# Optimization experiments

Hardware: AMD Instinct MI355X
Metric: run time of the kernel (lower is better)

## Reference

```python
import jax, jax.numpy as jnp
import numpy as np

B, P, N, H = 2, 512, 8, 32
INIT_RANGE = 0.02


def setup_inputs() -> dict:
    key = jax.random.key(0)
    k1, k2, k3 = jax.random.split(key, 3)
    d = jax.random.normal(k1, (B, P, N, H), dtype=jnp.float32)
    e = jax.random.normal(k2, (B, P, N, H), dtype=jnp.float32)
    W = jax.random.normal(k3, (N, H, H, H), dtype=jnp.float32) * INIT_RANGE
    return {"d": d, "e": e, "W": W}


def reference(d, e, W):
    # Trilinear contraction: v[b,p1,p2,n,h3] = sum_{h1,h2} d[b,p1,n,h1] e[b,p2,n,h2] W[n,h1,h2,h3]
    # Decompose into two batched matmuls to avoid the naive 4-way product:
    # tmp[b,p1,n,h2,h3] = sum_h1 d[b,p1,n,h1] W[n,h1,h2,h3]
    tmp = jnp.einsum('bpni,nijk->bpnjk', d, W)
    # v[b,p1,p2,n,h3] = sum_h2 tmp[b,p1,n,h2,h3] e[b,p2,n,h2]
    v = jnp.einsum('bpnjk,bqnj->bpqnk', tmp, e)
    return v
```

## Files before the change

kernel.cpp:

```cpp
#include <hip/hip_runtime.h>

#define BB 2
#define PP 512
#define NN 8
#define HH 32

typedef float f4     __attribute__((ext_vector_type(4)));
typedef float f32x4  __attribute__((ext_vector_type(4)));
typedef short bf16x8 __attribute__((ext_vector_type(8)));

__device__ __forceinline__ short f2bf(float f) {
  union { float f; unsigned u; } v; v.f = f;
  unsigned r = v.u + 0x7FFFu + ((v.u >> 16) & 1u);
  return (short)(r >> 16);
}

__global__ __launch_bounds__(256) void prep_kernel(
    const float* __restrict__ d, const float* __restrict__ W,
    short* __restrict__ tmpT) {
  const int bid    = blockIdx.x;
  const int b      = bid >> 9;
  const int rem    = bid & 511;
  const int n      = rem >> 6;
  const int p1base = (rem & 63) * 8;
  const int t      = threadIdx.x;

  __shared__ float dT[32][8];
  {
    const int h1 = t & 31, p1l = t >> 5;
    dT[h1][p1l] = d[(size_t)((b * PP + p1base + p1l) * NN + n) * HH + h1];
  }
  __syncthreads();

  const float* Wn = W + (size_t)n * HH * HH * HH;
  #pragma unroll
  for (int pp = 0; pp < 4; ++pp) {
    const int q  = pp * 256 + t;
    const int h3 = q & 31;
    const int h2 = q >> 5;
    float acc[8] = {0.f, 0.f, 0.f, 0.f, 0.f, 0.f, 0.f, 0.f};
    for (int h1 = 0; h1 < 32; ++h1) {
      const float w = Wn[h1 * 1024 + h2 * 32 + h3];
      const f4 a0 = *(const f4*)&dT[h1][0];
      const f4 a1 = *(const f4*)&dT[h1][4];
      acc[0] = fmaf(a0[0], w, acc[0]);
      acc[1] = fmaf(a0[1], w, acc[1]);
      acc[2] = fmaf(a0[2], w, acc[2]);
      acc[3] = fmaf(a0[3], w, acc[3]);
      acc[4] = fmaf(a1[0], w, acc[4]);
      acc[5] = fmaf(a1[1], w, acc[5]);
      acc[6] = fmaf(a1[2], w, acc[6]);
      acc[7] = fmaf(a1[3], w, acc[7]);
    }
    const size_t obase =
        ((size_t)(b * PP + p1base) * NN + n) * (HH * HH) + h3 * 32 + h2;
    #pragma unroll
    for (int p1l = 0; p1l < 8; ++p1l)
      tmpT[obase + (size_t)p1l * (NN * HH * HH)] = f2bf(acc[p1l]);
  }
}

__global__ __launch_bounds__(256) void ecvt_kernel(
    const float* __restrict__ e, short* __restrict__ eB) {
  const int i = (blockIdx.x * 256 + threadIdx.x) * 8;
  const f4 e0 = *(const f4*)(e + i);
  const f4 e1 = *(const f4*)(e + i + 4);
  bf16x8 v;
  v[0] = f2bf(e0[0]); v[1] = f2bf(e0[1]); v[2] = f2bf(e0[2]); v[3] = f2bf(e0[3]);
  v[4] = f2bf(e1[0]); v[5] = f2bf(e1[1]); v[6] = f2bf(e1[2]); v[7] = f2bf(e1[3]);
  *(bf16x8*)(eB + i) = v;
}

__global__ __launch_bounds__(256, 4) void vmain_kernel(
    const short* __restrict__ eB, const short* __restrict__ tmpT,
    float* __restrict__ out) {
  const int bid = blockIdx.x;
  const int b   = bid >> 9;
  const int p1  = bid & 511;
  const int t   = threadIdx.x;
  const int wv  = t >> 6;
  const int l   = t & 63;
  const int lr  = l & 15;
  const int lk  = l >> 4;

  bf16x8 bfr[8][2];
  const short* tb = tmpT + (size_t)(b * PP + p1) * (NN * HH * HH);
  #pragma unroll
  for (int n = 0; n < 8; ++n)
    #pragma unroll
    for (int c = 0; c < 2; ++c)
      bfr[n][c] = *(const bf16x8*)(tb + n * (HH * HH) + (c * 16 + lr) * 32 + lk * 8);

  const short* ebb  = eB + (size_t)b * (PP * NN * HH);
  float*       outb = out + (size_t)(b * PP + p1) * (PP * NN * HH);
  const f32x4  z    = {0.f, 0.f, 0.f, 0.f};

  for (int i = 0; i < 8; ++i) {
    const int m0 = (wv * 8 + i) * 16;
    #pragma unroll
    for (int n = 0; n < 8; ++n) {
      const bf16x8 a =
          *(const bf16x8*)(ebb + (size_t)((m0 + lr) * NN + n) * HH + lk * 8);
      const f32x4 c0 = __builtin_amdgcn_mfma_f32_16x16x32_bf16(bfr[n][0], a, z, 0, 0, 0);
      const f32x4 c1 = __builtin_amdgcn_mfma_f32_16x16x32_bf16(bfr[n][1], a, z, 0, 0, 0);
      float* op = outb + (size_t)(m0 + lr) * (NN * HH) + n * HH + lk * 4;
      *(f32x4*)op        = c0;
      *(f32x4*)(op + 16) = c1;
    }
  }
}

__device__ __forceinline__ void gemm_pv_f32e(const bf16x8 (&bfr)[8][2],
                                             const float* __restrict__ eb,
                                             float* __restrict__ outb,
                                             int wv, int lr, int lk) {
  for (int i = 0; i < 8; ++i) {
    const int m0 = (wv * 8 + i) * 16;
    #pragma unroll
    for (int n = 0; n < 8; ++n) {
      const float* ep = eb + (size_t)(((m0 + lr) * NN + n) * HH + lk * 8);
      const f4 e0 = *(const f4*)ep;
      const f4 e1 = *(const f4*)(ep + 4);
      bf16x8 a;
      a[0] = f2bf(e0[0]); a[1] = f2bf(e0[1]); a[2] = f2bf(e0[2]); a[3] = f2bf(e0[3]);
      a[4] = f2bf(e1[0]); a[5] = f2bf(e1[1]); a[6] = f2bf(e1[2]); a[7] = f2bf(e1[3]);
      const f32x4 z = {0.f, 0.f, 0.f, 0.f};
      const f32x4 c0 = __builtin_amdgcn_mfma_f32_16x16x32_bf16(bfr[n][0], a, z, 0, 0, 0);
      const f32x4 c1 = __builtin_amdgcn_mfma_f32_16x16x32_bf16(bfr[n][1], a, z, 0, 0, 0);
      float* op = outb + (size_t)(m0 + lr) * (NN * HH) + n * HH + lk * 4;
      *(f32x4*)op        = c0;
      *(f32x4*)(op + 16) = c1;
    }
  }
}

__global__ __launch_bounds__(256, 4) void fused_kernel(
    const float* __restrict__ d, const float* __restrict__ e,
    const float* __restrict__ W, float* __restrict__ out) {
  const int bid = blockIdx.x;
  const int b   = bid >> 9;
  const int p1  = bid & 511;
  const int t   = threadIdx.x;

  __shared__ float dsh[NN * HH];
  __shared__ short tsh[NN * HH * HH];
  dsh[t] = d[(size_t)(b * PP + p1) * (NN * HH) + t];
  __syncthreads();

  const int h3  = t & 31;
  const int h2b = t >> 5;
  for (int n = 0; n < 8; ++n) {
    f4 dv[8];
    #pragma unroll
    for (int j = 0; j < 8; ++j) dv[j] = *(const f4*)&dsh[n * 32 + j * 4];
    const float* Wn = W + (size_t)n * (HH * HH * HH);
    #pragma unroll
    for (int h2s = 0; h2s < 4; ++h2s) {
      const int h2 = h2s * 8 + h2b;
      float acc = 0.f;
      #pragma unroll
      for (int j = 0; j < 8; ++j)
        #pragma unroll
        for (int k = 0; k < 4; ++k)
          acc = fmaf(dv[j][k], Wn[(j * 4 + k) * 1024 + h2 * 32 + h3], acc);
      tsh[n * 1024 + h3 * 32 + h2] = f2bf(acc);
    }
  }
  __syncthreads();

  const int wv = t >> 6;
  const int l  = t & 63;
  const int lr = l & 15;
  const int lk = l >> 4;
  bf16x8 bfr[8][2];
  #pragma unroll
  for (int n = 0; n < 8; ++n)
    #pragma unroll
    for (int c = 0; c < 2; ++c)
      bfr[n][c] = *(const bf16x8*)&tsh[n * (HH * HH) + (c * 16 + lr) * 32 + lk * 8];

  gemm_pv_f32e(bfr, e + (size_t)b * (PP * NN * HH),
               out + (size_t)(b * PP + p1) * (PP * NN * HH), wv, lr, lk);
}

extern "C" void kernel_launch(void* const* d_in, const int* in_sizes, int n_in,
                              void* d_out, int out_size, void* d_ws, size_t ws_size,
                              hipStream_t stream) {
  const float* d = (const float*)d_in[0];
  const float* e = (const float*)d_in[1];
  const float* W = (const float*)d_in[2];
  float* out = (float*)d_out;

  const size_t tmp_bytes = (size_t)BB * PP * NN * HH * HH * sizeof(short);
  const size_t eb_bytes  = (size_t)BB * PP * NN * HH * sizeof(short);
  if (ws_size >= tmp_bytes + eb_bytes) {
    short* tmpT = (short*)d_ws;
    short* eB   = (short*)((char*)d_ws + tmp_bytes);
    prep_kernel<<<dim3(BB * NN * (PP / 8)), dim3(256), 0, stream>>>(d, W, tmpT);
    ecvt_kernel<<<dim3(BB * PP * NN * HH / (256 * 8)), dim3(256), 0, stream>>>(e, eB);
    vmain_kernel<<<dim3(BB * PP), dim3(256), 0, stream>>>(eB, tmpT, out);
  } else {
    fused_kernel<<<dim3(BB * PP), dim3(256), 0, stream>>>(d, e, W, out);
  }
}
```

Measured before the change: 151.3 us.

## Register-tile tmp precompute with transposed W and stage output stores through LDS

Adds a kernel that transposes W per (n,h1) slice so the tmp precompute can read eight contiguous h2 weights at once. Each thread then computes an 8x8 register tile (8 p1 values by 8 h2 values) and writes packed bf16x8 results instead of scattered 2-byte stores. The main MFMA kernel now stages its outputs through a swizzled LDS buffer, so each row is written to global memory as contiguous 512-byte segments rather than strided 16-byte chunks. In exchange it adds an extra launch, a larger workspace requirement, and extra LDS use that may lower occupancy.

```diff
diff --git a/kernel.cpp b/kernel.cpp
--- a/kernel.cpp
+++ b/kernel.cpp
@@ -15,48 +15,83 @@
   return (short)(r >> 16);
 }
 
-__global__ __launch_bounds__(256) void prep_kernel(
-    const float* __restrict__ d, const float* __restrict__ W,
+__global__ __launch_bounds__(256) void wtrans_kernel(
+    const float* __restrict__ W, float* __restrict__ WT) {
+  const int blk = blockIdx.x;
+  const int t   = threadIdx.x;
+  __shared__ float ls[32][33];
+  const float* src = W  + (size_t)blk * 1024;
+  float*       dst = WT + (size_t)blk * 1024;
+  #pragma unroll
+  for (int r = 0; r < 4; ++r) {
+    const int h2 = r * 8 + (t >> 5), h3 = t & 31;
+    ls[h2][h3] = src[h2 * 32 + h3];
+  }
+  __syncthreads();
+  #pragma unroll
+  for (int r = 0; r < 4; ++r) {
+    const int h3 = r * 8 + (t >> 5), h2 = t & 31;
+    dst[h3 * 32 + h2] = ls[h2][h3];
+  }
+}
+
+__global__ __launch_bounds__(256) void prep2_kernel(
+    const float* __restrict__ d, const float* __restrict__ WT,
     short* __restrict__ tmpT) {
   const int bid    = blockIdx.x;
-  const int b      = bid >> 9;
-  const int rem    = bid & 511;
-  const int n      = rem >> 6;
+  const int b      = bid >> 8;
+  const int rem    = bid & 255;
+  const int npair  = rem >> 6;
   const int p1base = (rem & 63) * 8;
   const int t      = threadIdx.x;
 
-  __shared__ float dT[32][8];
+  __shared__ float dsh[2][32][8];
   {
-    const int h1 = t & 31, p1l = t >> 5;
-    dT[h1][p1l] = d[(size_t)((b * PP + p1base + p1l) * NN + n) * HH + h1];
-  }
-  __syncthreads();
-
-  const float* Wn = W + (size_t)n * HH * HH * HH;
-  #pragma unroll
-  for (int pp = 0; pp < 4; ++pp) {
-    const int q  = pp * 256 + t;
-    const int h3 = q & 31;
-    const int h2 = q >> 5;
-    float acc[8] = {0.f, 0.f, 0.f, 0.f, 0.f, 0.f, 0.f, 0.f};
-    for (int h1 = 0; h1 < 32; ++h1) {
-      const float w = Wn[h1 * 1024 + h2 * 32 + h3];
-      const f4 a0 = *(const f4*)&dT[h1][0];
-      const f4 a1 = *(const f4*)&dT[h1][4];
-      acc[0] = fmaf(a0[0], w, acc[0]);
-      acc[1] = fmaf(a0[1], w, acc[1]);
-      acc[2] = fmaf(a0[2], w, acc[2]);
-      acc[3] = fmaf(a0[3], w, acc[3]);
-      acc[4] = fmaf(a1[0], w, acc[4]);
-      acc[5] = fmaf(a1[1], w, acc[5]);
-      acc[6] = fmaf(a1[2], w, acc[6]);
-      acc[7] = fmaf(a1[3], w, acc[7]);
-    }
-    const size_t obase =
-        ((size_t)(b * PP + p1base) * NN + n) * (HH * HH) + h3 * 32 + h2;
-    #pragma unroll
-    for (int p1l = 0; p1l < 8; ++p1l)
-      tmpT[obase + (size_t)p1l * (NN * HH * HH)] = f2bf(acc[p1l]);
+    const int h1 = t & 31, p1l = (t >> 5) & 7;
+    #pragma unroll
+    for (int r = 0; r < 2; ++r)
+      dsh[r][h1][p1l] =
+          d[(size_t)((b * PP + p1base + p1l) * NN + npair * 2 + r) * HH + h1];
+  }
+  __syncthreads();
+
+  const int np  = t >> 7;
+  const int h3  = (t >> 2) & 31;
+  const int h2g = t & 3;
+  const int n   = npair * 2 + np;
+
+  float acc[8][8];
+  #pragma unroll
+  for (int p = 0; p < 8; ++p)
+    #pragma unroll
+    for (int q = 0; q < 8; ++q) acc[p][q] = 0.f;
+
+  const float* wb = WT + ((size_t)(n * HH) * HH + h3) * HH + h2g * 8;
+  for (int h1 = 0; h1 < 32; ++h1) {
+    const f4 w0 = *(const f4*)(wb + (size_t)h1 * 1024);
+    const f4 w1 = *(const f4*)(wb + (size_t)h1 * 1024 + 4);
+    const f4 d0 = *(const f4*)&dsh[np][h1][0];
+    const f4 d1 = *(const f4*)&dsh[np][h1][4];
+    #pragma unroll
+    for (int p = 0; p < 4; ++p) {
+      #pragma unroll
+      for (int q = 0; q < 4; ++q) {
+        acc[p][q]         = fmaf(d0[p], w0[q], acc[p][q]);
+        acc[p][q + 4]     = fmaf(d0[p], w1[q], acc[p][q + 4]);
+        acc[p + 4][q]     = fmaf(d1[p], w0[q], acc[p + 4][q]);
+        acc[p + 4][q + 4] = fmaf(d1[p], w1[q], acc[p + 4][q + 4]);
+      }
+    }
+  }
+
+  const size_t obase =
+      ((size_t)(b * PP + p1base) * NN + n) * (HH * HH) + h3 * 32 + h2g * 8;
+  #pragma unroll
+  for (int p = 0; p < 8; ++p) {
+    bf16x8 v;
+    #pragma unroll
+    for (int q = 0; q < 8; ++q) v[q] = f2bf(acc[p][q]);
+    *(bf16x8*)(tmpT + obase + (size_t)p * (NN * HH * HH)) = v;
   }
 }
 
@@ -83,6 +118,9 @@
   const int lr  = l & 15;
   const int lk  = l >> 4;
 
+  __shared__ float lbuf[4][16][128];
+  float* wl = &lbuf[wv][0][0];
+
   bf16x8 bfr[8][2];
   const short* tb = tmpT + (size_t)(b * PP + p1) * (NN * HH * HH);
   #pragma unroll
@@ -98,22 +136,79 @@
   for (int i = 0; i < 8; ++i) {
     const int m0 = (wv * 8 + i) * 16;
     #pragma unroll
-    for (int n = 0; n < 8; ++n) {
-      const bf16x8 a =
-          *(const bf16x8*)(ebb + (size_t)((m0 + lr) * NN + n) * HH + lk * 8);
-      const f32x4 c0 = __builtin_amdgcn_mfma_f32_16x16x32_bf16(bfr[n][0], a, z, 0, 0, 0);
-      const f32x4 c1 = __builtin_amdgcn_mfma_f32_16x16x32_bf16(bfr[n][1], a, z, 0, 0, 0);
-      float* op = outb + (size_t)(m0 + lr) * (NN * HH) + n * HH + lk * 4;
-      *(f32x4*)op        = c0;
-      *(f32x4*)(op + 16) = c1;
-    }
-  }
-}
-
-__device__ __forceinline__ void gemm_pv_f32e(const bf16x8 (&bfr)[8][2],
-                                             const float* __restrict__ eb,
-                                             float* __restrict__ outb,
-                                             int wv, int lr, int lk) {
+    for (int half = 0; half < 2; ++half) {
+      const int n0 = half * 4;
+      #pragma unroll
+      for (int nn = 0; nn < 4; ++nn) {
+        const int n = n0 + nn;
+        const bf16x8 a =
+            *(const bf16x8*)(ebb + (size_t)((m0 + lr) * NN + n) * HH + lk * 8);
+        const f32x4 c0 = __builtin_amdgcn_mfma_f32_16x16x32_bf16(bfr[n][0], a, z, 0, 0, 0);
+        const f32x4 c1 = __builtin_amdgcn_mfma_f32_16x16x32_bf16(bfr[n][1], a, z, 0, 0, 0);
+        const int s0 = (nn * 8 + lk)     ^ (lr & 7);
+        const int s1 = (nn * 8 + 4 + lk) ^ (lr & 7);
+        *(f32x4*)(wl + lr * 128 + s0 * 4) = c0;
+        *(f32x4*)(wl + lr * 128 + s1 * 4) = c1;
+      }
+      #pragma unroll
+      for (int j = 0; j < 8; ++j) {
+        const int row  = 2 * j + (l >> 5);
+        const int slot = l & 31;
+        const f32x4 v = *(const f32x4*)(wl + row * 128 + ((slot ^ (row & 7)) * 4));
+        *(f32x4*)(outb + (size_t)(m0 + row) * (NN * HH) + n0 * HH + slot * 4) = v;
+      }
+    }
+  }
+}
+
+__global__ __launch_bounds__(256, 4) void fused_kernel(
+    const float* __restrict__ d, const float* __restrict__ e,
+    const float* __restrict__ W, float* __restrict__ out) {
+  const int bid = blockIdx.x;
+  const int b   = bid >> 9;
+  const int p1  = bid & 511;
+  const int t   = threadIdx.x;
+
+  __shared__ float dsh[NN * HH];
+  __shared__ short tsh[NN * HH * HH];
+  dsh[t] = d[(size_t)(b * PP + p1) * (NN * HH) + t];
+  __syncthreads();
+
+  const int h3  = t & 31;
+  const int h2b = t >> 5;
+  for (int n = 0; n < 8; ++n) {
+    f4 dv[8];
+    #pragma unroll
+    for (int j = 0; j < 8; ++j) dv[j] = *(const f4*)&dsh[n * 32 + j * 4];
+    const float* Wn = W + (size_t)n * (HH * HH * HH);
+    #pragma unroll
+    for (int h2s = 0; h2s < 4; ++h2s) {
+      const int h2 = h2s * 8 + h2b;
+      float acc = 0.f;
+      #pragma unroll
+      for (int j = 0; j < 8; ++j)
+        #pragma unroll
+        for (int k = 0; k < 4; ++k)
+          acc = fmaf(dv[j][k], Wn[(j * 4 + k) * 1024 + h2 * 32 + h3], acc);
+      tsh[n * 1024 + h3 * 32 + h2] = f2bf(acc);
+    }
+  }
+  __syncthreads();
+
+  const int wv = t >> 6;
+  const int l  = t & 63;
+  const int lr = l & 15;
+  const int lk = l >> 4;
+  bf16x8 bfr[8][2];
+  #pragma unroll
+  for (int n = 0; n < 8; ++n)
+    #pragma unroll
+    for (int c = 0; c < 2; ++c)
+      bfr[n][c] = *(const bf16x8*)&tsh[n * (HH * HH) + (c * 16 + lr) * 32 + lk * 8];
+
+  const float* eb   = e + (size_t)b * (PP * NN * HH);
+  float*       outb = out + (size_t)(b * PP + p1) * (PP * NN * HH);
+  const f32x4  z    = {0.f, 0.f, 0.f, 0.f};
   for (int i = 0; i < 8; ++i) {
     const int m0 = (wv * 8 + i) * 16;
     #pragma unroll
@@ -124,7 +219,6 @@
       bf16x8 a;
       a[0] = f2bf(e0[0]); a[1] = f2bf(e0[1]); a[2] = f2bf(e0[2]); a[3] = f2bf(e0[3]);
       a[4] = f2bf(e1[0]); a[5] = f2bf(e1[1]); a[6] = f2bf(e1[2]); a[7] = f2bf(e1[3]);
-      const f32x4 z = {0.f, 0.f, 0.f, 0.f};
       const f32x4 c0 = __builtin_amdgcn_mfma_f32_16x16x32_bf16(bfr[n][0], a, z, 0, 0, 0);
       const f32x4 c1 = __builtin_amdgcn_mfma_f32_16x16x32_bf16(bfr[n][1], a, z, 0, 0, 0);
       float* op = outb + (size_t)(m0 + lr) * (NN * HH) + n * HH + lk * 4;
@@ -132,55 +226,6 @@
       *(f32x4*)(op + 16) = c1;
     }
   }
-}
-
-__global__ __launch_bounds__(256, 4) void fused_kernel(
-    const float* __restrict__ d, const float* __restrict__ e,
-    const float* __restrict__ W, float* __restrict__ out) {
-  const int bid = blockIdx.x;
-  const int b   = bid >> 9;
-  const int p1  = bid & 511;
-  const int t   = threadIdx.x;
-
-  __shared__ float dsh[NN * HH];
-  __shared__ short tsh[NN * HH * HH];
-  dsh[t] = d[(size_t)(b * PP + p1) * (NN * HH) + t];
-  __syncthreads();
-
-  const int h3  = t & 31;
-  const int h2b = t >> 5;
-  for (int n = 0; n < 8; ++n) {
-    f4 dv[8];
-    #pragma unroll
-    for (int j = 0; j < 8; ++j) dv[j] = *(const f4*)&dsh[n * 32 + j * 4];
-    const float* Wn = W + (size_t)n * (HH * HH * HH);
-    #pragma unroll
-    for (int h2s = 0; h2s < 4; ++h2s) {
-      const int h2 = h2s * 8 + h2b;
-      float acc = 0.f;
-      #pragma unroll
-      for (int j = 0; j < 8; ++j)
-        #pragma unroll
-        for (int k = 0; k < 4; ++k)
-          acc = fmaf(dv[j][k], Wn[(j * 4 + k) * 1024 + h2 * 32 + h3], acc);
-      tsh[n * 1024 + h3 * 32 + h2] = f2bf(acc);
-    }
-  }
-  __syncthreads();
-
-  const int wv = t >> 6;
-  const int l  = t & 63;
-  const int lr = l & 15;
-  const int lk = l >> 4;
-  bf16x8 bfr[8][2];
-  #pragma unroll
-  for (int n = 0; n < 8; ++n)
-    #pragma unroll
-    for (int c = 0; c < 2; ++c)
-      bfr[n][c] = *(const bf16x8*)&tsh[n * (HH * HH) + (c * 16 + lr) * 32 + lk * 8];
-
-  gemm_pv_f32e(bfr, e + (size_t)b * (PP * NN * HH),
-               out + (size_t)(b * PP + p1) * (PP * NN * HH), wv, lr, lk);
 }
 
 extern "C" void kernel_launch(void* const* d_in, const int* in_sizes, int n_in,
@@ -193,11 +238,14 @@
 
   const size_t tmp_bytes = (size_t)BB * PP * NN * HH * HH * sizeof(short);
   const size_t eb_bytes  = (size_t)BB * PP * NN * HH * sizeof(short);
-  if (ws_size >= tmp_bytes + eb_bytes) {
+  const size_t wt_bytes  = (size_t)NN * HH * HH * HH * sizeof(float);
+  if (ws_size >= tmp_bytes + eb_bytes + wt_bytes) {
     short* tmpT = (short*)d_ws;
     short* eB   = (short*)((char*)d_ws + tmp_bytes);
-    prep_kernel<<<dim3(BB * NN * (PP / 8)), dim3(256), 0, stream>>>(d, W, tmpT);
+    float* WT   = (float*)((char*)d_ws + tmp_bytes + eb_bytes);
+    wtrans_kernel<<<dim3(NN * HH), dim3(256), 0, stream>>>(W, WT);
     ecvt_kernel<<<dim3(BB * PP * NN * HH / (256 * 8)), dim3(256), 0, stream>>>(e, eB);
+    prep2_kernel<<<dim3(BB * 4 * (PP / 8)), dim3(256), 0, stream>>>(d, WT, tmpT);
     vmain_kernel<<<dim3(BB * PP), dim3(256), 0, stream>>>(eB, tmpT, out);
   } else {
     fused_kernel<<<dim3(BB * PP), dim3(256), 0, stream>>>(d, e, W, out);
```

Measured after the change: 131.2 us. -13.3%, faster.
